# Kernel optimization log

Measured on AMD Instinct MI355X. Metric: run time of the kernel, lower is better.

Reference implementation:

```python
import jax, jax.numpy as jnp
import numpy as np

N_NODES = 50000
N_EDGES = 800000
D_IN, D_HID, D_OUT = 128, 256, 256


def _mean_agg(h_src, src, dst, n_nodes):
    # gather source features along edges, segment-sum into dst, divide by in-degree
    gathered = h_src[src]                                        # [E, d]
    sums = jax.ops.segment_sum(gathered, dst, num_segments=n_nodes)  # [N, d]
    deg = jax.ops.segment_sum(jnp.ones((src.shape[0],), h_src.dtype), dst,
                              num_segments=n_nodes)              # [N]
    return sums / jnp.clip(deg, 1.0)[:, None]


def setup_inputs() -> dict:
    key = jax.random.key(0)
    ks = jax.random.split(key, 10)
    s = 0.05
    return {
        "x": jax.random.normal(ks[0], (N_NODES, D_IN), jnp.float32),
        "src": jax.random.randint(ks[1], (N_EDGES,), 0, N_NODES, jnp.int32),
        "dst": jax.random.randint(ks[2], (N_EDGES,), 0, N_NODES, jnp.int32),
        "W_self1": jax.random.normal(ks[3], (D_IN, D_HID), jnp.float32) * s,
        "W_neigh1": jax.random.normal(ks[4], (D_IN, D_HID), jnp.float32) * s,
        "b1": jnp.zeros((D_HID,), jnp.float32),
        "W_self2": jax.random.normal(ks[5], (D_HID, D_OUT), jnp.float32) * s,
        "W_neigh2": jax.random.normal(ks[6], (D_HID, D_OUT), jnp.float32) * s,
        "b2": jnp.zeros((D_OUT,), jnp.float32),
        "W_res": jax.random.normal(ks[7], (D_IN, D_OUT), jnp.float32) * s,
        "W_mlp": jax.random.normal(ks[8], (D_OUT, 2), jnp.float32) * s,
        "b_mlp": jnp.zeros((2,), jnp.float32),
    }


def reference(x, src, dst, W_self1, W_neigh1, b1, W_self2, W_neigh2, b2,
              W_res, W_mlp, b_mlp):
    n = x.shape[0]
    # SAGEConv 1 (mean aggregator) + ReLU (dropout p=0.0 is identity)
    h = x @ W_self1 + _mean_agg(x, src, dst, n) @ W_neigh1 + b1
    h = jax.nn.relu(h)
    # SAGEConv 2
    h = h @ W_self2 + _mean_agg(h, src, dst, n) @ W_neigh2 + b2
    # residual connection
    h = h + x @ W_res
    # MLP head
    return h @ W_mlp + b_mlp
```

## Files before the change

### kernel.cpp

```cpp
#include <hip/hip_runtime.h>

#define N_NODES 50000
#define N_EDGES 800000
#define D_IN 128
#define D_HID 256
#define D_OUT 256

#define SCAN_BLOCKS ((N_NODES + 255) / 256)
#define NXB ((N_NODES + 127) / 128)
#define GEMM_GRID (NXB * 4)

using short8 = __attribute__((ext_vector_type(8))) short;
using f32x4  = __attribute__((ext_vector_type(4))) float;

__device__ inline unsigned short f2bf(float f) {
    unsigned u = __float_as_uint(f);
    u += 0x7fff + ((u >> 16) & 1);
    return (unsigned short)(u >> 16);
}
__device__ inline float bf2f(unsigned v16) {
    return __uint_as_float(v16 << 16);
}


__global__ void hist_kernel(const int* __restrict__ dst, int* __restrict__ cnt) {
    int e = blockIdx.x * blockDim.x + threadIdx.x;
    if (e < N_EDGES) atomicAdd(&cnt[dst[e]], 1);
}

__global__ __launch_bounds__(256) void scan1_kernel(const int* __restrict__ cnt,
                                                    int* __restrict__ blocksum) {
    int i = blockIdx.x * 256 + threadIdx.x;
    int v = (i < N_NODES) ? cnt[i] : 0;
    int lane = threadIdx.x & 63, wid = threadIdx.x >> 6;
    for (int off = 32; off; off >>= 1) v += __shfl_down(v, off);
    __shared__ int ws[4];
    if (lane == 0) ws[wid] = v;
    __syncthreads();
    if (threadIdx.x == 0) blocksum[blockIdx.x] = ws[0] + ws[1] + ws[2] + ws[3];
}

__global__ __launch_bounds__(256) void scan2_kernel(const int* __restrict__ blocksum,
                                                    int* __restrict__ blockoff) {
    int tid = threadIdx.x;
    int lane = tid & 63, wid = tid >> 6;
    int v = (tid < SCAN_BLOCKS) ? blocksum[tid] : 0;
    int inc = v;
    for (int off = 1; off < 64; off <<= 1) {
        int u = __shfl_up(inc, off);
        if (lane >= off) inc += u;
    }
    __shared__ int ws[4];
    if (lane == 63) ws[wid] = inc;
    __syncthreads();
    int base = 0;
    for (int w = 0; w < wid; ++w) base += ws[w];
    if (tid < SCAN_BLOCKS) blockoff[tid] = base + inc - v;
}

__global__ __launch_bounds__(256) void scan3_kernel(const int* __restrict__ cnt,
                                                    const int* __restrict__ blockoff,
                                                    int* __restrict__ row_ptr,
                                                    int* __restrict__ cursor,
                                                    float* __restrict__ inv_deg) {
    int i = blockIdx.x * 256 + threadIdx.x;
    int c = (i < N_NODES) ? cnt[i] : 0;
    int lane = threadIdx.x & 63, wid = threadIdx.x >> 6;
    int inc = c;
    for (int off = 1; off < 64; off <<= 1) {
        int u = __shfl_up(inc, off);
        if (lane >= off) inc += u;
    }
    __shared__ int ws[4];
    if (lane == 63) ws[wid] = inc;
    __syncthreads();
    int base = blockoff[blockIdx.x];
    for (int w = 0; w < wid; ++w) base += ws[w];
    if (i < N_NODES) {
        int pos = base + inc - c;
        row_ptr[i] = pos;
        cursor[i] = pos;
        inv_deg[i] = 1.0f / (float)max(c, 1);
    }
    if (i == 0) row_ptr[N_NODES] = N_EDGES;
}

__global__ void fill_kernel(const int* __restrict__ src, const int* __restrict__ dst,
                            int* __restrict__ cursor, int* __restrict__ srcs) {
    int e = blockIdx.x * blockDim.x + threadIdx.x;
    if (e < N_EDGES) {
        int pos = atomicAdd(&cursor[dst[e]], 1);
        srcs[pos] = src[e];
    }
}


__global__ void convx_kernel(const float* __restrict__ x,
                             unsigned short* __restrict__ A1,
                             unsigned short* __restrict__ A2) {
    int idx = blockIdx.x * 256 + threadIdx.x;
    if (idx >= N_NODES * D_IN) return;
    int n = idx >> 7, k = idx & 127;
    unsigned short b = f2bf(x[idx]);
    A1[(long)n * 256 + k] = b;
    A2[(long)n * 640 + 512 + k] = b;
}

__global__ void wconv1_kernel(const float* __restrict__ Ws, const float* __restrict__ Wn,
                              unsigned short* __restrict__ Wt) {
    int j = blockIdx.x;
    for (int k = threadIdx.x; k < 256; k += 256) {
        float v = (k < 128) ? Ws[k * 256 + j] : Wn[(k - 128) * 256 + j];
        Wt[j * 256 + k] = f2bf(v);
    }
}

__global__ void wconv2_kernel(const float* __restrict__ Ws, const float* __restrict__ Wn,
                              const float* __restrict__ Wr,
                              unsigned short* __restrict__ Wt) {
    int j = blockIdx.x;
    for (int k = threadIdx.x; k < 640; k += 256) {
        float v = (k < 256) ? Ws[k * 256 + j]
                : (k < 512) ? Wn[(k - 256) * 256 + j]
                            : Wr[(k - 512) * 256 + j];
        Wt[j * 640 + k] = f2bf(v);
    }
}


__global__ void agg1_kernel(const float* __restrict__ x,
                            const int* __restrict__ row_ptr,
                            const int* __restrict__ srcs,
                            const float* __restrict__ inv_deg,
                            unsigned short* __restrict__ A1) {
    int n = blockIdx.x;
    int tid = threadIdx.x;
    int beg = row_ptr[n], end = row_ptr[n + 1];
    float acc = 0.f;
    int e = beg;
    for (; e + 3 < end; e += 4) {
        int s0 = srcs[e], s1 = srcs[e + 1], s2 = srcs[e + 2], s3 = srcs[e + 3];
        float v0 = x[(long)s0 * D_IN + tid];
        float v1 = x[(long)s1 * D_IN + tid];
        float v2 = x[(long)s2 * D_IN + tid];
        float v3 = x[(long)s3 * D_IN + tid];
        acc += (v0 + v1) + (v2 + v3);
    }
    for (; e < end; ++e) acc += x[(long)srcs[e] * D_IN + tid];
    A1[(long)n * 256 + 128 + tid] = f2bf(acc * inv_deg[n]);
}

__global__ void agg2_kernel(unsigned short* __restrict__ A2,
                            const int* __restrict__ row_ptr,
                            const int* __restrict__ srcs,
                            const float* __restrict__ inv_deg) {
    int n = blockIdx.x;
    int tid = threadIdx.x;
    int beg = row_ptr[n], end = row_ptr[n + 1];
    float a0 = 0.f, a1 = 0.f;
    int e = beg;
    for (; e + 3 < end; e += 4) {
        int s0 = srcs[e], s1 = srcs[e + 1], s2 = srcs[e + 2], s3 = srcs[e + 3];
        unsigned v0 = ((const unsigned*)(A2 + (long)s0 * 640))[tid];
        unsigned v1 = ((const unsigned*)(A2 + (long)s1 * 640))[tid];
        unsigned v2 = ((const unsigned*)(A2 + (long)s2 * 640))[tid];
        unsigned v3 = ((const unsigned*)(A2 + (long)s3 * 640))[tid];
        a0 += (bf2f(v0 & 0xffffu) + bf2f(v1 & 0xffffu)) +
              (bf2f(v2 & 0xffffu) + bf2f(v3 & 0xffffu));
        a1 += (bf2f(v0 >> 16) + bf2f(v1 >> 16)) + (bf2f(v2 >> 16) + bf2f(v3 >> 16));
    }
    for (; e < end; ++e) {
        unsigned v = ((const unsigned*)(A2 + (long)srcs[e] * 640))[tid];
        a0 += bf2f(v & 0xffffu);
        a1 += bf2f(v >> 16);
    }
    float inv = inv_deg[n];
    unsigned o = (unsigned)f2bf(a0 * inv) | ((unsigned)f2bf(a1 * inv) << 16);
    ((unsigned*)(A2 + (long)n * 640 + 256))[tid] = o;
}


template <int K, bool RELU>
__global__ __launch_bounds__(256) void gemm_ldsb_kernel(
    const unsigned short* __restrict__ A, const unsigned short* __restrict__ Bt,
    const float* __restrict__ bias, unsigned short* __restrict__ out, int outStride) {
    constexpr int NC = K / 128;
    constexpr int NT = NC * 4;
    constexpr int LDSK = 132;
    __shared__ unsigned short Blds[2][64][LDSK];

    int tid = threadIdx.x;
    int lane = tid & 63, w = tid >> 6;
    int b = blockIdx.x;
    int xcd = b & 7, slot = b >> 3;
    int l = (xcd < 4) ? xcd * 196 + slot : 4 * 196 + (xcd - 4) * 195 + slot;
    int bx = l >> 2, by = l & 3;

    int rb = bx * 128 + w * 32;
    int cb = by * 64;
    int l15 = lane & 15;
    int kg = (lane >> 4) * 8;

    const unsigned short* pA[2];
#pragma unroll
    for (int i = 0; i < 2; ++i) {
        int r = rb + 16 * i + l15;
        if (r >= N_NODES) r = 0;
        pA[i] = A + (long)r * K + kg;
    }
    const unsigned short* pS[4];
    unsigned short* pW[4];
#pragma unroll
    for (int it = 0; it < 4; ++it) {
        int q = it * 256 + tid;
        int col = q >> 4, ck = q & 15;
        pS[it] = Bt + (long)(cb + col) * K + ck * 8;
        pW[it] = &Blds[0][col][ck * 8];
    }
    constexpr int BUFOFF = 64 * LDSK;

    short8 st[4];
#pragma unroll
    for (int it = 0; it < 4; ++it) st[it] = *(const short8*)(pS[it]);
#pragma unroll
    for (int it = 0; it < 4; ++it) *(short8*)(pW[it]) = st[it];
    __syncthreads();

    f32x4 acc[2][4] = {};
    short8 a0[2], a1[2];
#pragma unroll
    for (int i = 0; i < 2; ++i) a0[i] = *(const short8*)(pA[i]);

    for (int c = 0; c < NC; ++c) {
        int cur = c & 1;
        const unsigned short* Bb = &Blds[0][0][0] + cur * BUFOFF;
        bool more = (c + 1 < NC);
        if (more) {
#pragma unroll
            for (int it = 0; it < 4; ++it)
                st[it] = *(const short8*)(pS[it] + (c + 1) * 128);
        }
        int t0 = c * 4;
        {
#pragma unroll
            for (int i = 0; i < 2; ++i) a1[i] = *(const short8*)(pA[i] + (t0 + 1) * 32);
            short8 bfr[4];
#pragma unroll
            for (int j = 0; j < 4; ++j)
                bfr[j] = *(const short8*)(Bb + (16 * j + l15) * LDSK + 0 * 32 + kg);
#pragma unroll
            for (int i = 0; i < 2; ++i)
#pragma unroll
                for (int j = 0; j < 4; ++j)
                    acc[i][j] = __builtin_amdgcn_mfma_f32_16x16x32_bf16(a0[i], bfr[j], acc[i][j], 0, 0, 0);
        }
        {
#pragma unroll
            for (int i = 0; i < 2; ++i) a0[i] = *(const short8*)(pA[i] + (t0 + 2) * 32);
            short8 bfr[4];
#pragma unroll
            for (int j = 0; j < 4; ++j)
                bfr[j] = *(const short8*)(Bb + (16 * j + l15) * LDSK + 1 * 32 + kg);
#pragma unroll
            for (int i = 0; i < 2; ++i)
#pragma unroll
                for (int j = 0; j < 4; ++j)
                    acc[i][j] = __builtin_amdgcn_mfma_f32_16x16x32_bf16(a1[i], bfr[j], acc[i][j], 0, 0, 0);
        }
        {
#pragma unroll
            for (int i = 0; i < 2; ++i) a1[i] = *(const short8*)(pA[i] + (t0 + 3) * 32);
            short8 bfr[4];
#pragma unroll
            for (int j = 0; j < 4; ++j)
                bfr[j] = *(const short8*)(Bb + (16 * j + l15) * LDSK + 2 * 32 + kg);
#pragma unroll
            for (int i = 0; i < 2; ++i)
#pragma unroll
                for (int j = 0; j < 4; ++j)
                    acc[i][j] = __builtin_amdgcn_mfma_f32_16x16x32_bf16(a0[i], bfr[j], acc[i][j], 0, 0, 0);
        }
        {
            if (t0 + 4 < NT) {
#pragma unroll
                for (int i = 0; i < 2; ++i) a0[i] = *(const short8*)(pA[i] + (t0 + 4) * 32);
            }
            short8 bfr[4];
#pragma unroll
            for (int j = 0; j < 4; ++j)
                bfr[j] = *(const short8*)(Bb + (16 * j + l15) * LDSK + 3 * 32 + kg);
#pragma unroll
            for (int i = 0; i < 2; ++i)
#pragma unroll
                for (int j = 0; j < 4; ++j)
                    acc[i][j] = __builtin_amdgcn_mfma_f32_16x16x32_bf16(a1[i], bfr[j], acc[i][j], 0, 0, 0);
        }
        __syncthreads();
        if (more) {
#pragma unroll
            for (int it = 0; it < 4; ++it)
                *(short8*)(pW[it] + ((c + 1) & 1) * BUFOFF) = st[it];
        }
        __syncthreads();
    }

#pragma unroll
    for (int j = 0; j < 4; ++j) {
        int c = cb + 16 * j + l15;
        float bv = bias[c];
#pragma unroll
        for (int i = 0; i < 2; ++i) {
            int rbase = rb + 16 * i + (lane >> 4) * 4;
#pragma unroll
            for (int r = 0; r < 4; ++r) {
                int row = rbase + r;
                if (row < N_NODES) {
                    float v = acc[i][j][r] + bv;
                    if (RELU) v = fmaxf(v, 0.f);
                    out[(long)row * outStride + c] = f2bf(v);
                }
            }
        }
    }
}


__global__ __launch_bounds__(256) void head_kernel(const unsigned short* __restrict__ h2,
                                                   const float* __restrict__ Wmlp,
                                                   const float* __restrict__ bmlp,
                                                   float* __restrict__ out) {
    int n = blockIdx.x * 4 + (threadIdx.x >> 6);
    int lane = threadIdx.x & 63;
    const unsigned* p = (const unsigned*)(h2 + (long)n * 256 + lane * 4);
    unsigned v0 = p[0], v1 = p[1];
    float f0 = bf2f(v0 & 0xffffu), f1 = bf2f(v0 >> 16);
    float f2 = bf2f(v1 & 0xffffu), f3 = bf2f(v1 >> 16);
    int k = lane * 4;
    float p0 = f0 * Wmlp[k * 2]       + f1 * Wmlp[(k + 1) * 2]
             + f2 * Wmlp[(k + 2) * 2] + f3 * Wmlp[(k + 3) * 2];
    float p1 = f0 * Wmlp[k * 2 + 1]       + f1 * Wmlp[(k + 1) * 2 + 1]
             + f2 * Wmlp[(k + 2) * 2 + 1] + f3 * Wmlp[(k + 3) * 2 + 1];
    for (int off = 32; off; off >>= 1) {
        p0 += __shfl_down(p0, off);
        p1 += __shfl_down(p1, off);
    }
    if (lane == 0) {
        out[(long)n * 2]     = p0 + bmlp[0];
        out[(long)n * 2 + 1] = p1 + bmlp[1];
    }
}


extern "C" void kernel_launch(void* const* d_in, const int* in_sizes, int n_in,
                              void* d_out, int out_size, void* d_ws, size_t ws_size,
                              hipStream_t stream) {
    const float* x    = (const float*)d_in[0];
    const int*   src  = (const int*)d_in[1];
    const int*   dst  = (const int*)d_in[2];
    const float* Ws1  = (const float*)d_in[3];
    const float* Wn1  = (const float*)d_in[4];
    const float* b1   = (const float*)d_in[5];
    const float* Ws2  = (const float*)d_in[6];
    const float* Wn2  = (const float*)d_in[7];
    const float* b2   = (const float*)d_in[8];
    const float* Wres = (const float*)d_in[9];
    const float* Wmlp = (const float*)d_in[10];
    const float* bmlp = (const float*)d_in[11];
    float* out = (float*)d_out;

    char* ws = (char*)d_ws;
    size_t off = 0;
    auto alloc = [&](size_t bytes) {
        void* p = ws + off;
        off += (bytes + 255) & ~(size_t)255;
        return p;
    };
    int*            cnt      = (int*)alloc((size_t)N_NODES * 4);
    int*            row_ptr  = (int*)alloc((size_t)(N_NODES + 1) * 4);
    int*            cursor   = (int*)alloc((size_t)N_NODES * 4);
    float*          inv_deg  = (float*)alloc((size_t)N_NODES * 4);
    int*            srcs     = (int*)alloc((size_t)N_EDGES * 4);
    int*            blocksum = (int*)alloc((size_t)SCAN_BLOCKS * 4);
    int*            blockoff = (int*)alloc((size_t)SCAN_BLOCKS * 4);
    unsigned short* A1       = (unsigned short*)alloc((size_t)N_NODES * 256 * 2);
    unsigned short* A2       = (unsigned short*)alloc((size_t)N_NODES * 640 * 2);
    unsigned short* Wt1      = (unsigned short*)alloc((size_t)256 * 256 * 2);
    unsigned short* Wt2      = (unsigned short*)alloc((size_t)256 * 640 * 2);

    hipMemsetAsync(cnt, 0, (size_t)N_NODES * 4, stream);
    hist_kernel<<<(N_EDGES + 255) / 256, 256, 0, stream>>>(dst, cnt);
    scan1_kernel<<<SCAN_BLOCKS, 256, 0, stream>>>(cnt, blocksum);
    scan2_kernel<<<1, 256, 0, stream>>>(blocksum, blockoff);
    scan3_kernel<<<SCAN_BLOCKS, 256, 0, stream>>>(cnt, blockoff, row_ptr, cursor, inv_deg);
    fill_kernel<<<(N_EDGES + 255) / 256, 256, 0, stream>>>(src, dst, cursor, srcs);
    convx_kernel<<<(N_NODES * D_IN + 255) / 256, 256, 0, stream>>>(x, A1, A2);
    wconv1_kernel<<<256, 256, 0, stream>>>(Ws1, Wn1, Wt1);
    wconv2_kernel<<<256, 256, 0, stream>>>(Ws2, Wn2, Wres, Wt2);
    agg1_kernel<<<N_NODES, 128, 0, stream>>>(x, row_ptr, srcs, inv_deg, A1);

    gemm_ldsb_kernel<256, true><<<GEMM_GRID, 256, 0, stream>>>(A1, Wt1, b1, A2, 640);
    agg2_kernel<<<N_NODES, 128, 0, stream>>>(A2, row_ptr, srcs, inv_deg);
    gemm_ldsb_kernel<640, false><<<GEMM_GRID, 256, 0, stream>>>(A2, Wt2, b2, A1, 256);
    head_kernel<<<N_NODES / 4, 256, 0, stream>>>(A1, Wmlp, bmlp, out);
}
```

Measured before the change: 429.2 us.

## Gather bf16 x in agg1 and double-buffer whole A chunks in GEMM

The first aggregation now gathers neighbour features from the bf16 copy of x already stored in A1, instead of the fp32 x. This halves the bytes read per gathered row. The GEMM main loop is restructured to prefetch a full 128-wide K chunk of A into registers (two register sets, ping-pong), issuing global loads one chunk ahead of the MFMA work rather than one 32-wide slice ahead. This adds register pressure (16 short8 A fragments) that could reduce occupancy. The aggregation reads and writes A1 in the same kernel, but in disjoint column ranges.

```diff
diff --git a/kernel.cpp b/kernel.cpp
--- a/kernel.cpp
+++ b/kernel.cpp
@@ -128,8 +128,7 @@
 }
 
 
-__global__ void agg1_kernel(const float* __restrict__ x,
-                            const int* __restrict__ row_ptr,
+__global__ void agg1_kernel(const int* __restrict__ row_ptr,
                             const int* __restrict__ srcs,
                             const float* __restrict__ inv_deg,
                             unsigned short* __restrict__ A1) {
@@ -140,13 +139,13 @@
     int e = beg;
     for (; e + 3 < end; e += 4) {
         int s0 = srcs[e], s1 = srcs[e + 1], s2 = srcs[e + 2], s3 = srcs[e + 3];
-        float v0 = x[(long)s0 * D_IN + tid];
-        float v1 = x[(long)s1 * D_IN + tid];
-        float v2 = x[(long)s2 * D_IN + tid];
-        float v3 = x[(long)s3 * D_IN + tid];
-        acc += (v0 + v1) + (v2 + v3);
-    }
-    for (; e < end; ++e) acc += x[(long)srcs[e] * D_IN + tid];
+        unsigned v0 = A1[(long)s0 * 256 + tid];
+        unsigned v1 = A1[(long)s1 * 256 + tid];
+        unsigned v2 = A1[(long)s2 * 256 + tid];
+        unsigned v3 = A1[(long)s3 * 256 + tid];
+        acc += (bf2f(v0) + bf2f(v1)) + (bf2f(v2) + bf2f(v3));
+    }
+    for (; e < end; ++e) acc += bf2f((unsigned)A1[(long)srcs[e] * 256 + tid]);
     A1[(long)n * 256 + 128 + tid] = f2bf(acc * inv_deg[n]);
 }
 
@@ -185,7 +184,6 @@
     const unsigned short* __restrict__ A, const unsigned short* __restrict__ Bt,
     const float* __restrict__ bias, unsigned short* __restrict__ out, int outStride) {
     constexpr int NC = K / 128;
-    constexpr int NT = NC * 4;
     constexpr int LDSK = 132;
     __shared__ unsigned short Blds[2][64][LDSK];
 
@@ -219,95 +217,71 @@
     }
     constexpr int BUFOFF = 64 * LDSK;
 
+    f32x4 acc[2][4] = {};
     short8 st[4];
-#pragma unroll
-    for (int it = 0; it < 4; ++it) st[it] = *(const short8*)(pS[it]);
-#pragma unroll
-    for (int it = 0; it < 4; ++it) *(short8*)(pW[it]) = st[it];
+    short8 aA[8], aB[8];
+
+    auto stageIssue = [&](int cc) {
+#pragma unroll
+        for (int it = 0; it < 4; ++it) st[it] = *(const short8*)(pS[it] + cc * 128);
+    };
+    auto stageWrite = [&](int buf) {
+#pragma unroll
+        for (int it = 0; it < 4; ++it) *(short8*)(pW[it] + buf * BUFOFF) = st[it];
+    };
+    auto loadChunk = [&](short8 (&dst)[8], int cc) {
+#pragma unroll
+        for (int i = 0; i < 2; ++i)
+#pragma unroll
+            for (int t = 0; t < 4; ++t)
+                dst[i * 4 + t] = *(const short8*)(pA[i] + (cc * 4 + t) * 32);
+    };
+    auto computeChunk = [&](const short8 (&areg)[8], int buf) {
+        const unsigned short* Bb = &Blds[0][0][0] + buf * BUFOFF;
+#pragma unroll
+        for (int t = 0; t < 4; ++t) {
+            short8 bfr[4];
+#pragma unroll
+            for (int j = 0; j < 4; ++j)
+                bfr[j] = *(const short8*)(Bb + (16 * j + l15) * LDSK + t * 32 + kg);
+#pragma unroll
+            for (int i = 0; i < 2; ++i)
+#pragma unroll
+                for (int j = 0; j < 4; ++j)
+                    acc[i][j] = __builtin_amdgcn_mfma_f32_16x16x32_bf16(
+                        areg[i * 4 + t], bfr[j], acc[i][j], 0, 0, 0);
+        }
+    };
+
+    stageIssue(0);
+    stageWrite(0);
+    loadChunk(aA, 0);
     __syncthreads();
 
-    f32x4 acc[2][4] = {};
-    short8 a0[2], a1[2];
-#pragma unroll
-    for (int i = 0; i < 2; ++i) a0[i] = *(const short8*)(pA[i]);
-
-    for (int c = 0; c < NC; ++c) {
-        int cur = c & 1;
-        const unsigned short* Bb = &Blds[0][0][0] + cur * BUFOFF;
-        bool more = (c + 1 < NC);
-        if (more) {
-#pragma unroll
-            for (int it = 0; it < 4; ++it)
-                st[it] = *(const short8*)(pS[it] + (c + 1) * 128);
+    int c = 0;
+    while (c + 2 <= NC) {
+        stageIssue(c + 1);
+        loadChunk(aB, c + 1);
+        computeChunk(aA, c & 1);
+        __syncthreads();
+        stageWrite((c + 1) & 1);
+        __syncthreads();
+        if (c + 2 < NC) {
+            stageIssue(c + 2);
+            loadChunk(aA, c + 2);
         }
-        int t0 = c * 4;
-        {
-#pragma unroll
-            for (int i = 0; i < 2; ++i) a1[i] = *(const short8*)(pA[i] + (t0 + 1) * 32);
-            short8 bfr[4];
-#pragma unroll
-            for (int j = 0; j < 4; ++j)
-                bfr[j] = *(const short8*)(Bb + (16 * j + l15) * LDSK + 0 * 32 + kg);
-#pragma unroll
-            for (int i = 0; i < 2; ++i)
-#pragma unroll
-                for (int j = 0; j < 4; ++j)
-                    acc[i][j] = __builtin_amdgcn_mfma_f32_16x16x32_bf16(a0[i], bfr[j], acc[i][j], 0, 0, 0);
-        }
-        {
-#pragma unroll
-            for (int i = 0; i < 2; ++i) a0[i] = *(const short8*)(pA[i] + (t0 + 2) * 32);
-            short8 bfr[4];
-#pragma unroll
-            for (int j = 0; j < 4; ++j)
-                bfr[j] = *(const short8*)(Bb + (16 * j + l15) * LDSK + 1 * 32 + kg);
-#pragma unroll
-            for (int i = 0; i < 2; ++i)
-#pragma unroll
-                for (int j = 0; j < 4; ++j)
-                    acc[i][j] = __builtin_amdgcn_mfma_f32_16x16x32_bf16(a1[i], bfr[j], acc[i][j], 0, 0, 0);
-        }
-        {
-#pragma unroll
-            for (int i = 0; i < 2; ++i) a1[i] = *(const short8*)(pA[i] + (t0 + 3) * 32);
-            short8 bfr[4];
-#pragma unroll
-            for (int j = 0; j < 4; ++j)
-                bfr[j] = *(const short8*)(Bb + (16 * j + l15) * LDSK + 2 * 32 + kg);
-#pragma unroll
-            for (int i = 0; i < 2; ++i)
-#pragma unroll
-                for (int j = 0; j < 4; ++j)
-                    acc[i][j] = __builtin_amdgcn_mfma_f32_16x16x32_bf16(a0[i], bfr[j], acc[i][j], 0, 0, 0);
-        }
-        {
-            if (t0 + 4 < NT) {
-#pragma unroll
-                for (int i = 0; i < 2; ++i) a0[i] = *(const short8*)(pA[i] + (t0 + 4) * 32);
-            }
-            short8 bfr[4];
-#pragma unroll
-            for (int j = 0; j < 4; ++j)
-                bfr[j] = *(const short8*)(Bb + (16 * j + l15) * LDSK + 3 * 32 + kg);
-#pragma unroll
-            for (int i = 0; i < 2; ++i)
-#pragma unroll
-                for (int j = 0; j < 4; ++j)
-                    acc[i][j] = __builtin_amdgcn_mfma_f32_16x16x32_bf16(a1[i], bfr[j], acc[i][j], 0, 0, 0);
-        }
+        computeChunk(aB, (c + 1) & 1);
         __syncthreads();
-        if (more) {
-#pragma unroll
-            for (int it = 0; it < 4; ++it)
-                *(short8*)(pW[it] + ((c + 1) & 1) * BUFOFF) = st[it];
-        }
+        if (c + 2 < NC) stageWrite((c + 2) & 1);
         __syncthreads();
-    }
+        c += 2;
+    }
+    if (c < NC) computeChunk(aA, c & 1);
 
 #pragma unroll
     for (int j = 0; j < 4; ++j) {
-        int c = cb + 16 * j + l15;
-        float bv = bias[c];
+        int cc = cb + 16 * j + l15;
+        float bv = bias[cc];
 #pragma unroll
         for (int i = 0; i < 2; ++i) {
             int rbase = rb + 16 * i + (lane >> 4) * 4;
@@ -317,7 +291,7 @@
                 if (row < N_NODES) {
                     float v = acc[i][j][r] + bv;
                     if (RELU) v = fmaxf(v, 0.f);
-                    out[(long)row * outStride + c] = f2bf(v);
+                    out[(long)row * outStride + cc] = f2bf(v);
                 }
             }
         }
@@ -396,7 +370,7 @@
     convx_kernel<<<(N_NODES * D_IN + 255) / 256, 256, 0, stream>>>(x, A1, A2);
     wconv1_kernel<<<256, 256, 0, stream>>>(Ws1, Wn1, Wt1);
     wconv2_kernel<<<256, 256, 0, stream>>>(Ws2, Wn2, Wres, Wt2);
-    agg1_kernel<<<N_NODES, 128, 0, stream>>>(x, row_ptr, srcs, inv_deg, A1);
+    agg1_kernel<<<N_NODES, 128, 0, stream>>>(row_ptr, srcs, inv_deg, A1);
 
     gemm_ldsb_kernel<256, true><<<GEMM_GRID, 256, 0, stream>>>(A1, Wt1, b1, A2, 640);
     agg2_kernel<<<N_NODES, 128, 0, stream>>>(A2, row_ptr, srcs, inv_deg);
```

Measured after the change: 414.5 us. 3.4% less time.
